# Kernel optimization log

Measured on AMD Instinct MI355X. Metric: run time of the kernel, lower is better.

The kernel has to match this reference:

```python
import jax, jax.numpy as jnp
import numpy as np

B, P, E = 16, 1024, 768
HID, HEADS = 768, 12
DH = HID // HEADS  # 64
EPS = 1e-5


def setup_inputs() -> dict:
    key = jax.random.key(0)
    ks = jax.random.split(key, 4)
    return {
        "x": jax.random.normal(ks[0], (B, P, E), dtype=jnp.float32),
        "ln_weight": jnp.ones((P, E), dtype=jnp.float32),
        "ln_bias": jnp.zeros((P, E), dtype=jnp.float32),
        "qkv": jax.random.normal(ks[1], (E, 3 * HID), dtype=jnp.float32),
        "lin_w": jax.random.normal(ks[2], (HID, E), dtype=jnp.float32) * 0.02,
        "lin_b": jax.random.normal(ks[3], (E,), dtype=jnp.float32) * 0.02,
    }


def reference(x, ln_weight, ln_bias, qkv, lin_w, lin_b):
    # LayerNorm over the last TWO dims (patches, emb), per torch nn.LayerNorm((P, E))
    mean = jnp.mean(x, axis=(-2, -1), keepdims=True)
    var = jnp.var(x, axis=(-2, -1), keepdims=True)
    xn = (x - mean) / jnp.sqrt(var + EPS) * ln_weight + ln_bias

    # QKV projection: [B,P,E] @ [E,3*HID] -> [B,P,3*HID]
    proj = xn @ qkv
    # view(B,P,heads,-1) then permute -> [B,heads,P,3*DH]; chunk along last dim
    proj = proj.reshape(B, P, HEADS, 3 * DH).transpose(0, 2, 1, 3)
    q, k, v = proj[..., :DH], proj[..., DH:2 * DH], proj[..., 2 * DH:]

    # Softmax-free attention: (Q K^T) V
    atten = jnp.einsum("bhqd,bhkd->bhqk", q, k)  # [B,H,P,P]
    out = jnp.einsum("bhqk,bhkd->bhqd", atten, v)  # [B,H,P,DH]

    out = out.transpose(0, 2, 1, 3).reshape(B, P, HID)
    # dropout p=0.0 (eval) -> identity
    out = jax.nn.relu(out @ lin_w + lin_b)
    return out + x
```

## Files before the change

### kernel.cpp

```cpp
#include <hip/hip_runtime.h>
#include <hip/hip_bf16.h>
#include <cstdint>

#define BB   16
#define PP   1024
#define EE   768
#define HID  768
#define NH   12
#define DH   64
#define NPB  (PP * EE)
#define MROWS (BB * PP)

typedef __bf16 bf16_t;
typedef __bf16 bf16x8 __attribute__((ext_vector_type(8)));
typedef float  f32x4  __attribute__((ext_vector_type(4)));

__device__ __forceinline__ void gld16(const void* g, void* l) {
    __builtin_amdgcn_global_load_lds(
        (const __attribute__((address_space(1))) void*)(uintptr_t)g,
        (__attribute__((address_space(3))) void*)(uint32_t)(uintptr_t)l,
        16, 0, 0);
}

__global__ __launch_bounds__(256) void stats1_kernel(const float* __restrict__ x,
                                                     float* __restrict__ part) {
    int bid = blockIdx.x;
    int b = bid >> 6, s = bid & 63;
    const float4* xp = (const float4*)(x + (size_t)b * NPB + (size_t)s * 12288);
    float sum = 0.f, ss = 0.f;
#pragma unroll
    for (int i = 0; i < 12; ++i) {
        float4 v = xp[i * 256 + threadIdx.x];
        sum += v.x + v.y + v.z + v.w;
        ss  += v.x * v.x + v.y * v.y + v.z * v.z + v.w * v.w;
    }
#pragma unroll
    for (int off = 32; off > 0; off >>= 1) {
        sum += __shfl_down(sum, off, 64);
        ss  += __shfl_down(ss,  off, 64);
    }
    __shared__ float tmp[8];
    int wave = threadIdx.x >> 6, lane = threadIdx.x & 63;
    if (lane == 0) { tmp[wave * 2] = sum; tmp[wave * 2 + 1] = ss; }
    __syncthreads();
    if (threadIdx.x == 0) {
        part[bid * 2]     = tmp[0] + tmp[2] + tmp[4] + tmp[6];
        part[bid * 2 + 1] = tmp[1] + tmp[3] + tmp[5] + tmp[7];
    }
}

__global__ __launch_bounds__(256) void prep_kernel(const float* __restrict__ qkvw,
                                                   const float* __restrict__ linw,
                                                   const float* __restrict__ part,
                                                   bf16_t* __restrict__ qkvT,
                                                   bf16_t* __restrict__ lwT,
                                                   float* __restrict__ stats) {
    int bid = blockIdx.x;
    if (bid < 576) {
        __shared__ float lds[64][65];
        const float* src; bf16_t* dst; int r0, c0, W;
        if (bid < 432) {
            int tr = bid / 36, tc = bid - tr * 36;
            r0 = tr * 64; c0 = tc * 64; src = qkvw; W = 2304; dst = qkvT;
        } else {
            int bb = bid - 432;
            int tr = bb / 12, tc = bb - tr * 12;
            r0 = tr * 64; c0 = tc * 64; src = linw; W = 768; dst = lwT;
        }
        int t = threadIdx.x;
        int rr = t >> 4, cc4 = (t & 15) * 4;
#pragma unroll
        for (int j = 0; j < 4; ++j) {
            float4 v = *(const float4*)(src + (size_t)(r0 + rr + j * 16) * W + c0 + cc4);
            lds[rr + j * 16][cc4 + 0] = v.x;
            lds[rr + j * 16][cc4 + 1] = v.y;
            lds[rr + j * 16][cc4 + 2] = v.z;
            lds[rr + j * 16][cc4 + 3] = v.w;
        }
        __syncthreads();
        int cl = t >> 3, rgl = (t & 7) * 8;
#pragma unroll
        for (int jj = 0; jj < 2; ++jj) {
            int c = jj * 32 + cl;
            union { bf16_t h[8]; uint4 u; } o;
#pragma unroll
            for (int k = 0; k < 8; ++k) o.h[k] = (bf16_t)lds[rgl + k][c];
            *(uint4*)(dst + (size_t)(c0 + c) * 768 + r0 + rgl) = o.u;
        }
    } else {
        int wave = threadIdx.x >> 6, lane = threadIdx.x & 63;
#pragma unroll
        for (int j = 0; j < 4; ++j) {
            int b = wave * 4 + j;
            float sum = part[(b * 64 + lane) * 2];
            float ss  = part[(b * 64 + lane) * 2 + 1];
#pragma unroll
            for (int off = 32; off > 0; off >>= 1) {
                sum += __shfl_down(sum, off, 64);
                ss  += __shfl_down(ss,  off, 64);
            }
            if (lane == 0) {
                const float inv_n = 1.f / (float)NPB;
                float mean = sum * inv_n;
                float var  = ss * inv_n - mean * mean;
                stats[b * 2]     = mean;
                stats[b * 2 + 1] = rsqrtf(var + 1e-5f);
            }
        }
    }
}

__global__ __launch_bounds__(256) void ln_apply_kernel(const float* __restrict__ x,
                                                       const float* __restrict__ lnw,
                                                       const float* __restrict__ lnb,
                                                       const float* __restrict__ stats,
                                                       bf16_t* __restrict__ xn) {
    int i = (blockIdx.x * 256 + threadIdx.x) * 8;
    int b = i / NPB;
    int r = i - b * NPB;
    float mean = stats[b * 2], rstd = stats[b * 2 + 1];
    float4 x0 = *(const float4*)(x + i),     x1 = *(const float4*)(x + i + 4);
    float4 w0 = *(const float4*)(lnw + r),   w1 = *(const float4*)(lnw + r + 4);
    float4 c0 = *(const float4*)(lnb + r),   c1 = *(const float4*)(lnb + r + 4);
    union { bf16_t h[8]; uint4 u; } o;
    o.h[0] = (bf16_t)((x0.x - mean) * rstd * w0.x + c0.x);
    o.h[1] = (bf16_t)((x0.y - mean) * rstd * w0.y + c0.y);
    o.h[2] = (bf16_t)((x0.z - mean) * rstd * w0.z + c0.z);
    o.h[3] = (bf16_t)((x0.w - mean) * rstd * w0.w + c0.w);
    o.h[4] = (bf16_t)((x1.x - mean) * rstd * w1.x + c1.x);
    o.h[5] = (bf16_t)((x1.y - mean) * rstd * w1.y + c1.y);
    o.h[6] = (bf16_t)((x1.z - mean) * rstd * w1.z + c1.z);
    o.h[7] = (bf16_t)((x1.w - mean) * rstd * w1.w + c1.w);
    *(uint4*)(xn + i) = o.u;
}

template <int KDIM>
__device__ __forceinline__ void gemm_core_128(const bf16_t* __restrict__ A,
                                              const bf16_t* __restrict__ Bt,
                                              int mBase, int nBase,
                                              f32x4 acc[4][4],
                                              bf16_t* As, bf16_t* Bs) {
    const int t = threadIdx.x;
    const int lane = t & 63, wave = t >> 6;
    const int wm = wave >> 1, wn = wave & 1;
    const int m16 = lane & 15, quad = lane >> 4;

    const int sr = t >> 3, s8 = t & 7;
    const bf16_t* pa[4]; const bf16_t* pb[4];
#pragma unroll
    for (int i = 0; i < 4; ++i) {
        int row = i * 32 + sr;
        int g = (s8 - (row & 7)) & 7;
        pa[i] = A  + (size_t)(mBase + row) * KDIM + g * 8;
        pb[i] = Bt + (size_t)(nBase + row) * KDIM + g * 8;
    }

    int raOff[4][2], rbOff[4][2];
#pragma unroll
    for (int i = 0; i < 4; ++i) {
        int ra = wm * 64 + i * 16 + m16;
        int rb = wn * 64 + i * 16 + m16;
#pragma unroll
        for (int ks = 0; ks < 2; ++ks) {
            raOff[i][ks] = ra * 64 + (((ks * 4 + quad) + (ra & 7)) & 7) * 8;
            rbOff[i][ks] = rb * 64 + (((ks * 4 + quad) + (rb & 7)) & 7) * 8;
        }
    }

    const f32x4 z = {0.f, 0.f, 0.f, 0.f};
#pragma unroll
    for (int mm = 0; mm < 4; ++mm)
#pragma unroll
        for (int nn = 0; nn < 4; ++nn) acc[mm][nn] = z;

    for (int k0 = 0; k0 < KDIM; k0 += 64) {
        __syncthreads();
#pragma unroll
        for (int i = 0; i < 4; ++i) {
            gld16(pa[i] + k0, As + i * 2048 + t * 8);
            gld16(pb[i] + k0, Bs + i * 2048 + t * 8);
        }
        __syncthreads();
#pragma unroll
        for (int ks = 0; ks < 2; ++ks) {
            bf16x8 af[4], bfv[4];
#pragma unroll
            for (int i = 0; i < 4; ++i) {
                af[i]  = *(const bf16x8*)(As + raOff[i][ks]);
                bfv[i] = *(const bf16x8*)(Bs + rbOff[i][ks]);
            }
#pragma unroll
            for (int mm = 0; mm < 4; ++mm)
#pragma unroll
                for (int nn = 0; nn < 4; ++nn)
                    acc[mm][nn] = __builtin_amdgcn_mfma_f32_16x16x32_bf16(
                        af[mm], bfv[nn], acc[mm][nn], 0, 0, 0);
        }
    }
}

#define MFMA_PHASE(AF, BF, MO, NO)                                           \
    do {                                                                     \
        __builtin_amdgcn_s_setprio(1);                                       \
        _Pragma("unroll") for (int mf2 = 0; mf2 < 4; ++mf2)                  \
        _Pragma("unroll") for (int nf2 = 0; nf2 < 2; ++nf2)                  \
        _Pragma("unroll") for (int ks2 = 0; ks2 < 2; ++ks2)                  \
            acc[(MO) + mf2][(NO) + nf2] =                                    \
                __builtin_amdgcn_mfma_f32_16x16x32_bf16(                     \
                    AF[mf2][ks2], BF[nf2][ks2],                              \
                    acc[(MO) + mf2][(NO) + nf2], 0, 0, 0);                   \
        __builtin_amdgcn_s_setprio(0);                                       \
    } while (0)

__global__ __launch_bounds__(512, 2) void gemm_qkv_kernel(const bf16_t* __restrict__ xn,
                                                          const bf16_t* __restrict__ qkvT,
                                                          bf16_t* __restrict__ q,
                                                          bf16_t* __restrict__ kt,
                                                          bf16_t* __restrict__ vt) {
    __shared__ bf16_t smem[65536];
    const int t = threadIdx.x, lane = t & 63, wave = t >> 6;
    const int wm = wave >> 2, wn = wave & 3;
    const int m16 = lane & 15, quad = lane >> 4;

    const int lb = blockIdx.y * 9 + blockIdx.x;
    const int id = (lb & 7) * 72 + (lb >> 3);
    const int tx = id % 9, ty = id / 9;
    const int mBase = ty * 256, nBase = tx * 256;

    const int sr = t >> 3, s8 = t & 7;
    const int g8 = (s8 - (sr & 7)) & 7;
    const bf16_t* pa = xn   + (size_t)(mBase + sr) * 768 + g8 * 8;
    const bf16_t* pb = qkvT + (size_t)(nBase + sr) * 768 + g8 * 8;

    const int ch0 = ((quad + (m16 & 7)) & 7) * 8;
    const int ch1 = (((4 + quad) + (m16 & 7)) & 7) * 8;
    const int aBase = wm * 8192 + m16 * 64;
    const int bBase = 16384 + (wn >> 1) * 8192 + ((wn & 1) * 64 + m16) * 64;

    f32x4 acc[8][4];
    const f32x4 z = {0.f, 0.f, 0.f, 0.f};
#pragma unroll
    for (int mm = 0; mm < 8; ++mm)
#pragma unroll
        for (int nn = 0; nn < 4; ++nn) acc[mm][nn] = z;

#pragma unroll
    for (int i = 0; i < 4; ++i) {
        gld16(pa + (size_t)i * 49152, smem + i * 4096 + t * 8);
        gld16(pb + (size_t)i * 49152, smem + 16384 + i * 4096 + t * 8);
    }
    __syncthreads();

#pragma unroll
    for (int ktile = 0; ktile < 12; ++ktile) {
        const int par = (ktile & 1) << 15;
        const int nxt = ((ktile + 1) & 1) << 15;
        bf16x8 a0[4][2], a1[4][2], b0[2][2], b1[2][2];
        if (ktile + 1 < 12) {
#pragma unroll
            for (int i = 0; i < 4; ++i) {
                gld16(pa + (size_t)i * 49152 + (ktile + 1) * 64,
                      smem + nxt + i * 4096 + t * 8);
                gld16(pb + (size_t)i * 49152 + (ktile + 1) * 64,
                      smem + nxt + 16384 + i * 4096 + t * 8);
            }
        }
#pragma unroll
        for (int mf = 0; mf < 4; ++mf) {
            a0[mf][0] = *(const bf16x8*)(smem + par + aBase + mf * 1024 + ch0);
            a0[mf][1] = *(const bf16x8*)(smem + par + aBase + mf * 1024 + ch1);
        }
#pragma unroll
        for (int nf = 0; nf < 2; ++nf) {
            b0[nf][0] = *(const bf16x8*)(smem + par + bBase + nf * 1024 + ch0);
            b0[nf][1] = *(const bf16x8*)(smem + par + bBase + nf * 1024 + ch1);
        }
        MFMA_PHASE(a0, b0, 0, 0);
        __builtin_amdgcn_s_barrier();
#pragma unroll
        for (int nf = 0; nf < 2; ++nf) {
            b1[nf][0] = *(const bf16x8*)(smem + par + bBase + (2 + nf) * 1024 + ch0);
            b1[nf][1] = *(const bf16x8*)(smem + par + bBase + (2 + nf) * 1024 + ch1);
        }
        MFMA_PHASE(a0, b1, 0, 2);
        __builtin_amdgcn_s_barrier();
#pragma unroll
        for (int mf = 0; mf < 4; ++mf) {
            a1[mf][0] = *(const bf16x8*)(smem + par + aBase + (4 + mf) * 1024 + ch0);
            a1[mf][1] = *(const bf16x8*)(smem + par + aBase + (4 + mf) * 1024 + ch1);
        }
        MFMA_PHASE(a1, b0, 4, 0);
        __builtin_amdgcn_s_barrier();
        MFMA_PHASE(a1, b1, 4, 2);
        __syncthreads();
    }

    bf16_t* slot = smem + wave * 8192;
    const int g64 = tx * 4 + wn;
    const int cls = g64 % 3, h = g64 / 3;
    const int b = mBase >> 10, p0 = mBase & 1023;
    const int rowTile = p0 + wm * 128;

    if (cls == 0) {
#pragma unroll
        for (int pass = 0; pass < 2; ++pass) {
#pragma unroll
            for (int mf2 = 0; mf2 < 4; ++mf2)
#pragma unroll
                for (int nf = 0; nf < 4; ++nf)
#pragma unroll
                    for (int i = 0; i < 4; ++i)
                        slot[(mf2 * 16 + quad * 4 + i) * 72 + nf * 16 + m16] =
                            (bf16_t)acc[pass * 4 + mf2][nf][i];
            asm volatile("s_waitcnt lgkmcnt(0)" ::: "memory");
            __builtin_amdgcn_sched_barrier(0);
#pragma unroll
            for (int j = 0; j < 8; ++j) {
                int r = j * 8 + (lane >> 3), cc = lane & 7;
                bf16x8 val = *(const bf16x8*)(slot + r * 72 + cc * 8);
                *(bf16x8*)(q + ((size_t)(b * 1024 + rowTile + pass * 64 + r)) * 768 +
                           h * 64 + cc * 8) = val;
            }
            if (pass == 0) {
                asm volatile("s_waitcnt lgkmcnt(0)" ::: "memory");
                __builtin_amdgcn_sched_barrier(0);
            }
        }
    } else {
        bf16_t* dst = (cls == 1) ? kt : vt;
        const size_t bh = (size_t)(b * 12 + h);
#pragma unroll
        for (int pass = 0; pass < 2; ++pass) {
#pragma unroll
            for (int mf2 = 0; mf2 < 4; ++mf2)
#pragma unroll
                for (int nf = 0; nf < 4; ++nf) {
                    int c = nf * 16 + m16;
                    union { bf16_t hh[4]; uint2 u; } pk;
#pragma unroll
                    for (int i = 0; i < 4; ++i)
                        pk.hh[i] = (bf16_t)acc[pass * 4 + mf2][nf][i];
                    *(uint2*)(slot + c * 72 + mf2 * 16 + quad * 4) = pk.u;
                }
            asm volatile("s_waitcnt lgkmcnt(0)" ::: "memory");
            __builtin_amdgcn_sched_barrier(0);
#pragma unroll
            for (int j = 0; j < 8; ++j) {
                int c = (lane >> 3) + j * 8, r8 = (lane & 7) * 8;
                bf16x8 val = *(const bf16x8*)(slot + c * 72 + r8);
                *(bf16x8*)(dst + (bh * 64 + c) * 1024 + p0 + wm * 128 +
                           pass * 64 + r8) = val;
            }
            if (pass == 0) {
                asm volatile("s_waitcnt lgkmcnt(0)" ::: "memory");
                __builtin_amdgcn_sched_barrier(0);
            }
        }
    }
}

__global__ __launch_bounds__(256) void kv_kernel(const bf16_t* __restrict__ kt,
                                                 const bf16_t* __restrict__ vt,
                                                 bf16_t* __restrict__ thi,
                                                 bf16_t* __restrict__ tlo) {
    __shared__ float red[4 * 64 * 65];
    const int bh = blockIdx.x;
    const bf16_t* Kb = kt + (size_t)bh * DH * PP;
    const bf16_t* Vb = vt + (size_t)bh * DH * PP;
    const int t = threadIdx.x;
    const int lane = t & 63, wave = t >> 6;
    const int m16 = lane & 15, quad = lane >> 4;
    const f32x4 z = {0.f, 0.f, 0.f, 0.f};
    f32x4 acc[4][4];
#pragma unroll
    for (int mm = 0; mm < 4; ++mm)
#pragma unroll
        for (int nn = 0; nn < 4; ++nn) acc[mm][nn] = z;

    for (int ks = 0; ks < 8; ++ks) {
        int kb = wave * 256 + ks * 32 + quad * 8;
        bf16x8 af[4], bfv[4];
#pragma unroll
        for (int mm = 0; mm < 4; ++mm)
            af[mm] = *(const bf16x8*)(Kb + (size_t)(mm * 16 + m16) * PP + kb);
#pragma unroll
        for (int nn = 0; nn < 4; ++nn)
            bfv[nn] = *(const bf16x8*)(Vb + (size_t)(nn * 16 + m16) * PP + kb);
#pragma unroll
        for (int mm = 0; mm < 4; ++mm)
#pragma unroll
            for (int nn = 0; nn < 4; ++nn)
                acc[mm][nn] = __builtin_amdgcn_mfma_f32_16x16x32_bf16(
                    af[mm], bfv[nn], acc[mm][nn], 0, 0, 0);
    }
#pragma unroll
    for (int mm = 0; mm < 4; ++mm)
#pragma unroll
        for (int nn = 0; nn < 4; ++nn)
#pragma unroll
            for (int i = 0; i < 4; ++i)
                red[wave * 4160 + (mm * 16 + quad * 4 + i) * 65 + nn * 16 + m16] =
                    acc[mm][nn][i];
    __syncthreads();
#pragma unroll
    for (int j = 0; j < 16; ++j) {
        int idx = j * 256 + t;
        int m = idx >> 6, n = idx & 63;
        int a = m * 65 + n;
        float s = red[a] + red[4160 + a] + red[8320 + a] + red[12480 + a];
        bf16_t hi = (bf16_t)s;
        float lo = s - (float)hi;
        thi[(size_t)bh * 4096 + idx] = hi;
        tlo[(size_t)bh * 4096 + idx] = (bf16_t)lo;
    }
}

__global__ __launch_bounds__(256) void u_kernel(const bf16_t* __restrict__ thi,
                                                const bf16_t* __restrict__ tlo,
                                                const bf16_t* __restrict__ lwT,
                                                bf16_t* __restrict__ ut) {
    const int bh = blockIdx.x;
    const int b = bh / NH, h = bh - b * NH;
    const int nBase = blockIdx.y * 256;
    const bf16_t* Th = thi + (size_t)bh * 4096;
    const bf16_t* Tl = tlo + (size_t)bh * 4096;
    const int t = threadIdx.x, lane = t & 63, wave = t >> 6;
    const int wm = wave >> 1, wn = wave & 1;
    const int m16 = lane & 15, quad = lane >> 4;
    const f32x4 z = {0.f, 0.f, 0.f, 0.f};
    f32x4 acc[2][8];
#pragma unroll
    for (int mm = 0; mm < 2; ++mm)
#pragma unroll
        for (int nn = 0; nn < 8; ++nn) acc[mm][nn] = z;

#pragma unroll
    for (int ks = 0; ks < 2; ++ks) {
        bf16x8 ah[2], al[2], bfr[8];
#pragma unroll
        for (int mm = 0; mm < 2; ++mm) {
            ah[mm] = *(const bf16x8*)(Th + (wm * 32 + mm * 16 + m16) * 64 + ks * 32 + quad * 8);
            al[mm] = *(const bf16x8*)(Tl + (wm * 32 + mm * 16 + m16) * 64 + ks * 32 + quad * 8);
        }
#pragma unroll
        for (int nn = 0; nn < 8; ++nn)
            bfr[nn] = *(const bf16x8*)(
                lwT + (size_t)(nBase + wn * 128 + nn * 16 + m16) * 768 + h * 64 + ks * 32 + quad * 8);
#pragma unroll
        for (int mm = 0; mm < 2; ++mm)
#pragma unroll
            for (int nn = 0; nn < 8; ++nn) {
                acc[mm][nn] = __builtin_amdgcn_mfma_f32_16x16x32_bf16(
                    ah[mm], bfr[nn], acc[mm][nn], 0, 0, 0);
                acc[mm][nn] = __builtin_amdgcn_mfma_f32_16x16x32_bf16(
                    al[mm], bfr[nn], acc[mm][nn], 0, 0, 0);
            }
    }
#pragma unroll
    for (int mm = 0; mm < 2; ++mm)
#pragma unroll
        for (int nn = 0; nn < 8; ++nn) {
            int e  = nBase + wn * 128 + nn * 16 + m16;
            int d1 = wm * 32 + mm * 16 + quad * 4;
            union { bf16_t hh[4]; uint2 u; } pk;
#pragma unroll
            for (int i = 0; i < 4; ++i) pk.hh[i] = (bf16_t)acc[mm][nn][i];
            *(uint2*)(ut + ((size_t)b * 768 + e) * 768 + h * 64 + d1) = pk.u;
        }
}

__global__ __launch_bounds__(256) void gemm_out_kernel(const bf16_t* __restrict__ q,
                                                       const bf16_t* __restrict__ ut,
                                                       const float* __restrict__ linb,
                                                       const float* __restrict__ x,
                                                       float* __restrict__ out) {
    __shared__ bf16_t smem[16384];
    f32x4 acc[4][4];
    const int lb  = blockIdx.y * 6 + blockIdx.x;
    const int swz = (lb & 7) * 96 + (lb >> 3);
    const int tx  = swz % 6, ty = swz / 6;
    const int mBase = ty * 128, nBase = tx * 128;
    const int b = mBase >> 10;
    gemm_core_128<768>(q, ut + (size_t)b * 768 * 768, mBase, nBase, acc,
                       smem, smem + 8192);

    const int lane = threadIdx.x & 63, wave = threadIdx.x >> 6;
    const int wm = wave >> 1, wn = wave & 1;
    const int m16 = lane & 15, quad = lane >> 4;
#pragma unroll
    for (int mm = 0; mm < 4; ++mm) {
#pragma unroll
        for (int i = 0; i < 4; ++i) {
            size_t row = mBase + wm * 64 + mm * 16 + quad * 4 + i;
#pragma unroll
            for (int nn = 0; nn < 4; ++nn) {
                int col = nBase + wn * 64 + nn * 16 + m16;
                float v = acc[mm][nn][i] + linb[col];
                v = fmaxf(v, 0.f) + x[row * EE + col];
                out[row * EE + col] = v;
            }
        }
    }
}

extern "C" void kernel_launch(void* const* d_in, const int* in_sizes, int n_in,
                              void* d_out, int out_size, void* d_ws, size_t ws_size,
                              hipStream_t stream) {
    const float* x    = (const float*)d_in[0];
    const float* lnw  = (const float*)d_in[1];
    const float* lnb  = (const float*)d_in[2];
    const float* qkvw = (const float*)d_in[3];
    const float* linw = (const float*)d_in[4];
    const float* linb = (const float*)d_in[5];
    float* out = (float*)d_out;
    char* ws = (char*)d_ws;

    float*  part  = (float*)(ws + 0);
    float*  stats = (float*)(ws + 8192);
    bf16_t* xn    = (bf16_t*)(ws + 8448);
    bf16_t* qkvT  = (bf16_t*)(ws + 25174272);
    bf16_t* lwT   = (bf16_t*)(ws + 28713216);
    bf16_t* q     = (bf16_t*)(ws + 29892864);
    bf16_t* kt    = (bf16_t*)(ws + 55058688);
    bf16_t* vt    = (bf16_t*)(ws + 80224512);
    bf16_t* thi   = qkvT;
    bf16_t* tlo   = qkvT + 192 * 4096;
    bf16_t* ut    = kt;

    stats1_kernel<<<dim3(BB * 64), dim3(256), 0, stream>>>(x, part);
    prep_kernel<<<dim3(577), dim3(256), 0, stream>>>(qkvw, linw, part, qkvT, lwT, stats);
    ln_apply_kernel<<<dim3(6144), dim3(256), 0, stream>>>(x, lnw, lnb, stats, xn);
    gemm_qkv_kernel<<<dim3(9, 64), dim3(512), 0, stream>>>(xn, qkvT, q, kt, vt);
    kv_kernel<<<dim3(192), dim3(256), 0, stream>>>(kt, vt, thi, tlo);
    u_kernel<<<dim3(192, 3), dim3(256), 0, stream>>>(thi, tlo, lwT, ut);
    gemm_out_kernel<<<dim3(6, 128), dim3(256), 0, stream>>>(q, ut, linb, x, out);
}
```

Before: 260.5 us.

## Retile QKV GEMM to 128x256 blocks with 256 threads and K=32 steps

The QKV projection GEMM drops from 256x256 tiles with 8 waves to 128x256 tiles with 4 waves (2x2 wave grid, each wave 64x128). The K step shrinks from 64 to 32, which cuts shared memory from 128KB to 48KB so more blocks can be resident and the grid doubles to 1152 blocks. The shared-memory swizzle, load mapping and epilogue are reworked to match. Smaller tiles lower the arithmetic intensity per block, and there are twice as many K iterations, each with barriers.

```diff
diff --git a/kernel.cpp b/kernel.cpp
--- a/kernel.cpp
+++ b/kernel.cpp
@@ -199,148 +199,138 @@
     }
 }
 
-#define MFMA_PHASE(AF, BF, MO, NO)                                           \
-    do {                                                                     \
-        __builtin_amdgcn_s_setprio(1);                                       \
-        _Pragma("unroll") for (int mf2 = 0; mf2 < 4; ++mf2)                  \
-        _Pragma("unroll") for (int nf2 = 0; nf2 < 2; ++nf2)                  \
-        _Pragma("unroll") for (int ks2 = 0; ks2 < 2; ++ks2)                  \
-            acc[(MO) + mf2][(NO) + nf2] =                                    \
-                __builtin_amdgcn_mfma_f32_16x16x32_bf16(                     \
-                    AF[mf2][ks2], BF[nf2][ks2],                              \
-                    acc[(MO) + mf2][(NO) + nf2], 0, 0, 0);                   \
-        __builtin_amdgcn_s_setprio(0);                                       \
-    } while (0)
-
-__global__ __launch_bounds__(512, 2) void gemm_qkv_kernel(const bf16_t* __restrict__ xn,
+__global__ __launch_bounds__(256, 2) void gemm_qkv_kernel(const bf16_t* __restrict__ xn,
                                                           const bf16_t* __restrict__ qkvT,
                                                           bf16_t* __restrict__ q,
                                                           bf16_t* __restrict__ kt,
                                                           bf16_t* __restrict__ vt) {
-    __shared__ bf16_t smem[65536];
+    __shared__ bf16_t smem[24576];
     const int t = threadIdx.x, lane = t & 63, wave = t >> 6;
-    const int wm = wave >> 2, wn = wave & 3;
+    const int wm = wave >> 1, wn = wave & 1;
     const int m16 = lane & 15, quad = lane >> 4;
 
     const int lb = blockIdx.y * 9 + blockIdx.x;
-    const int id = (lb & 7) * 72 + (lb >> 3);
+    const int id = (lb & 7) * 144 + (lb >> 3);
     const int tx = id % 9, ty = id / 9;
-    const int mBase = ty * 256, nBase = tx * 256;
-
-    const int sr = t >> 3, s8 = t & 7;
-    const int g8 = (s8 - (sr & 7)) & 7;
-    const bf16_t* pa = xn   + (size_t)(mBase + sr) * 768 + g8 * 8;
-    const bf16_t* pb = qkvT + (size_t)(nBase + sr) * 768 + g8 * 8;
-
-    const int ch0 = ((quad + (m16 & 7)) & 7) * 8;
-    const int ch1 = (((4 + quad) + (m16 & 7)) & 7) * 8;
-    const int aBase = wm * 8192 + m16 * 64;
-    const int bBase = 16384 + (wn >> 1) * 8192 + ((wn & 1) * 64 + m16) * 64;
-
-    f32x4 acc[8][4];
+    const int mBase = ty * 128, nBase = tx * 256;
+
+    const bf16_t* gsrc[6];
+    int ldst[6];
+#pragma unroll
+    for (int j = 0; j < 2; ++j) {
+        int c = t + 256 * j;
+        int l = c >> 3, lg = ((c & 7) - (l & 7)) & 7;
+        gsrc[j] = xn + (size_t)(mBase + l + (lg >> 2) * 64) * 768 + (lg & 3) * 8;
+        ldst[j] = c * 8;
+    }
+#pragma unroll
+    for (int j = 0; j < 4; ++j) {
+        int c = t + 256 * j;
+        int l = c >> 3, lg = ((c & 7) - (l & 7)) & 7;
+        gsrc[2 + j] = qkvT + (size_t)(nBase + l + (lg >> 2) * 128) * 768 + (lg & 3) * 8;
+        ldst[2 + j] = 4096 + c * 8;
+    }
+
+    int aOff[4], bOff[8];
+#pragma unroll
+    for (int mf = 0; mf < 4; ++mf)
+        aOff[mf] = (mf * 16 + m16) * 64 + (((wm * 4 + quad) + (m16 & 7)) & 7) * 8;
+#pragma unroll
+    for (int nf = 0; nf < 8; ++nf)
+        bOff[nf] = 4096 + (nf * 16 + m16) * 64 + (((wn * 4 + quad) + (m16 & 7)) & 7) * 8;
+
+    f32x4 acc[4][8];
     const f32x4 z = {0.f, 0.f, 0.f, 0.f};
 #pragma unroll
-    for (int mm = 0; mm < 8; ++mm)
-#pragma unroll
-        for (int nn = 0; nn < 4; ++nn) acc[mm][nn] = z;
-
-#pragma unroll
-    for (int i = 0; i < 4; ++i) {
-        gld16(pa + (size_t)i * 49152, smem + i * 4096 + t * 8);
-        gld16(pb + (size_t)i * 49152, smem + 16384 + i * 4096 + t * 8);
-    }
+    for (int mf = 0; mf < 4; ++mf)
+#pragma unroll
+        for (int nf = 0; nf < 8; ++nf) acc[mf][nf] = z;
+
+#pragma unroll
+    for (int j = 0; j < 6; ++j) gld16(gsrc[j], smem + ldst[j]);
     __syncthreads();
 
 #pragma unroll
-    for (int ktile = 0; ktile < 12; ++ktile) {
-        const int par = (ktile & 1) << 15;
-        const int nxt = ((ktile + 1) & 1) << 15;
-        bf16x8 a0[4][2], a1[4][2], b0[2][2], b1[2][2];
-        if (ktile + 1 < 12) {
-#pragma unroll
-            for (int i = 0; i < 4; ++i) {
-                gld16(pa + (size_t)i * 49152 + (ktile + 1) * 64,
-                      smem + nxt + i * 4096 + t * 8);
-                gld16(pb + (size_t)i * 49152 + (ktile + 1) * 64,
-                      smem + nxt + 16384 + i * 4096 + t * 8);
-            }
-        }
-#pragma unroll
-        for (int mf = 0; mf < 4; ++mf) {
-            a0[mf][0] = *(const bf16x8*)(smem + par + aBase + mf * 1024 + ch0);
-            a0[mf][1] = *(const bf16x8*)(smem + par + aBase + mf * 1024 + ch1);
-        }
-#pragma unroll
-        for (int nf = 0; nf < 2; ++nf) {
-            b0[nf][0] = *(const bf16x8*)(smem + par + bBase + nf * 1024 + ch0);
-            b0[nf][1] = *(const bf16x8*)(smem + par + bBase + nf * 1024 + ch1);
-        }
-        MFMA_PHASE(a0, b0, 0, 0);
-        __builtin_amdgcn_s_barrier();
-#pragma unroll
-        for (int nf = 0; nf < 2; ++nf) {
-            b1[nf][0] = *(const bf16x8*)(smem + par + bBase + (2 + nf) * 1024 + ch0);
-            b1[nf][1] = *(const bf16x8*)(smem + par + bBase + (2 + nf) * 1024 + ch1);
-        }
-        MFMA_PHASE(a0, b1, 0, 2);
-        __builtin_amdgcn_s_barrier();
-#pragma unroll
-        for (int mf = 0; mf < 4; ++mf) {
-            a1[mf][0] = *(const bf16x8*)(smem + par + aBase + (4 + mf) * 1024 + ch0);
-            a1[mf][1] = *(const bf16x8*)(smem + par + aBase + (4 + mf) * 1024 + ch1);
-        }
-        MFMA_PHASE(a1, b0, 4, 0);
-        __builtin_amdgcn_s_barrier();
-        MFMA_PHASE(a1, b1, 4, 2);
-        __syncthreads();
-    }
-
-    bf16_t* slot = smem + wave * 8192;
-    const int g64 = tx * 4 + wn;
-    const int cls = g64 % 3, h = g64 / 3;
+    for (int it = 0; it < 12; ++it) {
+#pragma unroll
+        for (int s = 0; s < 2; ++s) {
+            const int step = it * 2 + s;
+            const int par = s * 12288, nxt = 12288 - par;
+            if (step < 23) {
+                const int kq = (step + 1) * 32;
+#pragma unroll
+                for (int j = 0; j < 6; ++j)
+                    gld16(gsrc[j] + kq, smem + nxt + ldst[j]);
+            }
+            bf16x8 af[4], bf0[4], bf1[4];
+#pragma unroll
+            for (int mf = 0; mf < 4; ++mf)
+                af[mf] = *(const bf16x8*)(smem + par + aOff[mf]);
+#pragma unroll
+            for (int nf = 0; nf < 4; ++nf)
+                bf0[nf] = *(const bf16x8*)(smem + par + bOff[nf]);
+            __builtin_amdgcn_s_setprio(1);
+#pragma unroll
+            for (int mf = 0; mf < 4; ++mf)
+#pragma unroll
+                for (int nf = 0; nf < 4; ++nf)
+                    acc[mf][nf] = __builtin_amdgcn_mfma_f32_16x16x32_bf16(
+                        af[mf], bf0[nf], acc[mf][nf], 0, 0, 0);
+            __builtin_amdgcn_s_setprio(0);
+            __builtin_amdgcn_s_barrier();
+#pragma unroll
+            for (int nf = 0; nf < 4; ++nf)
+                bf1[nf] = *(const bf16x8*)(smem + par + bOff[4 + nf]);
+            __builtin_amdgcn_s_setprio(1);
+#pragma unroll
+            for (int mf = 0; mf < 4; ++mf)
+#pragma unroll
+                for (int nf = 0; nf < 4; ++nf)
+                    acc[mf][4 + nf] = __builtin_amdgcn_mfma_f32_16x16x32_bf16(
+                        af[mf], bf1[nf], acc[mf][4 + nf], 0, 0, 0);
+            __builtin_amdgcn_s_setprio(0);
+            __syncthreads();
+        }
+    }
+
+    bf16_t* slot = smem + wave * 4608;
     const int b = mBase >> 10, p0 = mBase & 1023;
-    const int rowTile = p0 + wm * 128;
-
-    if (cls == 0) {
-#pragma unroll
-        for (int pass = 0; pass < 2; ++pass) {
-#pragma unroll
-            for (int mf2 = 0; mf2 < 4; ++mf2)
-#pragma unroll
-                for (int nf = 0; nf < 4; ++nf)
+
+#pragma unroll
+    for (int half = 0; half < 2; ++half) {
+        const int g64 = tx * 4 + wn * 2 + half;
+        const int cls = g64 % 3, h = g64 / 3;
+        if (cls == 0) {
+#pragma unroll
+            for (int mf = 0; mf < 4; ++mf)
+#pragma unroll
+                for (int nfl = 0; nfl < 4; ++nfl)
 #pragma unroll
                     for (int i = 0; i < 4; ++i)
-                        slot[(mf2 * 16 + quad * 4 + i) * 72 + nf * 16 + m16] =
-                            (bf16_t)acc[pass * 4 + mf2][nf][i];
+                        slot[(mf * 16 + quad * 4 + i) * 72 + nfl * 16 + m16] =
+                            (bf16_t)acc[mf][half * 4 + nfl][i];
             asm volatile("s_waitcnt lgkmcnt(0)" ::: "memory");
             __builtin_amdgcn_sched_barrier(0);
 #pragma unroll
             for (int j = 0; j < 8; ++j) {
                 int r = j * 8 + (lane >> 3), cc = lane & 7;
                 bf16x8 val = *(const bf16x8*)(slot + r * 72 + cc * 8);
-                *(bf16x8*)(q + ((size_t)(b * 1024 + rowTile + pass * 64 + r)) * 768 +
+                *(bf16x8*)(q + ((size_t)(b * 1024 + p0 + wm * 64 + r)) * 768 +
                            h * 64 + cc * 8) = val;
             }
-            if (pass == 0) {
-                asm volatile("s_waitcnt lgkmcnt(0)" ::: "memory");
-                __builtin_amdgcn_sched_barrier(0);
-            }
-        }
-    } else {
-        bf16_t* dst = (cls == 1) ? kt : vt;
-        const size_t bh = (size_t)(b * 12 + h);
-#pragma unroll
-        for (int pass = 0; pass < 2; ++pass) {
-#pragma unroll
-            for (int mf2 = 0; mf2 < 4; ++mf2)
-#pragma unroll
-                for (int nf = 0; nf < 4; ++nf) {
-                    int c = nf * 16 + m16;
+        } else {
+            bf16_t* dst = (cls == 1) ? kt : vt;
+            const size_t bh = (size_t)(b * 12 + h);
+#pragma unroll
+            for (int mf = 0; mf < 4; ++mf)
+#pragma unroll
+                for (int nfl = 0; nfl < 4; ++nfl) {
+                    int c = nfl * 16 + m16;
                     union { bf16_t hh[4]; uint2 u; } pk;
 #pragma unroll
                     for (int i = 0; i < 4; ++i)
-                        pk.hh[i] = (bf16_t)acc[pass * 4 + mf2][nf][i];
-                    *(uint2*)(slot + c * 72 + mf2 * 16 + quad * 4) = pk.u;
+                        pk.hh[i] = (bf16_t)acc[mf][half * 4 + nfl][i];
+                    *(uint2*)(slot + c * 72 + mf * 16 + quad * 4) = pk.u;
                 }
             asm volatile("s_waitcnt lgkmcnt(0)" ::: "memory");
             __builtin_amdgcn_sched_barrier(0);
@@ -348,13 +338,12 @@
             for (int j = 0; j < 8; ++j) {
                 int c = (lane >> 3) + j * 8, r8 = (lane & 7) * 8;
                 bf16x8 val = *(const bf16x8*)(slot + c * 72 + r8);
-                *(bf16x8*)(dst + (bh * 64 + c) * 1024 + p0 + wm * 128 +
-                           pass * 64 + r8) = val;
-            }
-            if (pass == 0) {
-                asm volatile("s_waitcnt lgkmcnt(0)" ::: "memory");
-                __builtin_amdgcn_sched_barrier(0);
-            }
+                *(bf16x8*)(dst + (bh * 64 + c) * 1024 + p0 + wm * 64 + r8) = val;
+            }
+        }
+        if (half == 0) {
+            asm volatile("s_waitcnt lgkmcnt(0)" ::: "memory");
+            __builtin_amdgcn_sched_barrier(0);
         }
     }
 }
@@ -530,7 +519,7 @@
     stats1_kernel<<<dim3(BB * 64), dim3(256), 0, stream>>>(x, part);
     prep_kernel<<<dim3(577), dim3(256), 0, stream>>>(qkvw, linw, part, qkvT, lwT, stats);
     ln_apply_kernel<<<dim3(6144), dim3(256), 0, stream>>>(x, lnw, lnb, stats, xn);
-    gemm_qkv_kernel<<<dim3(9, 64), dim3(512), 0, stream>>>(xn, qkvT, q, kt, vt);
+    gemm_qkv_kernel<<<dim3(9, 128), dim3(256), 0, stream>>>(xn, qkvT, q, kt, vt);
     kv_kernel<<<dim3(192), dim3(256), 0, stream>>>(kt, vt, thi, tlo);
     u_kernel<<<dim3(192, 3), dim3(256), 0, stream>>>(thi, tlo, lwT, ut);
     gemm_out_kernel<<<dim3(6, 128), dim3(256), 0, stream>>>(q, ut, linb, x, out);
```

New measurement: 261.0 us. About the same (+0.2%).
